# Performance work log

Measured on AMD Instinct MI355X. Metric: run time of the kernel, lower is better.

Reference implementation:

```python
import jax, jax.numpy as jnp
import numpy as np

B, S, D_MODEL, H = 2, 2048, 1024, 16
D_K = D_MODEL // H
THETA = 10000.0


def setup_inputs() -> dict:
    key = jax.random.key(0)
    k1, k2, k3 = jax.random.split(key, 3)
    x = jax.random.normal(k1, (B, S, D_MODEL), dtype=jnp.float32)
    token_positions = jnp.tile(jnp.arange(S, dtype=jnp.int32), (B, 1))
    qkv_w = jax.random.normal(k2, (3 * D_MODEL, D_MODEL), dtype=jnp.float32) * (D_MODEL ** -0.5)
    out_w = jax.random.normal(k3, (D_MODEL, D_MODEL), dtype=jnp.float32) * (D_MODEL ** -0.5)
    return {"x": x, "token_positions": token_positions, "qkv_w": qkv_w, "out_w": out_w}


def _apply_rope(t, pos):
    # t: [B, H, S, d_k], pos: [B, S]
    half = D_K // 2
    inv_freq = THETA ** (-jnp.arange(0, half, dtype=jnp.float32) * 2.0 / D_K)  # [half]
    ang = pos.astype(jnp.float32)[:, None, :, None] * inv_freq  # [B,1,S,half]
    cos, sin = jnp.cos(ang), jnp.sin(ang)
    t1 = t[..., 0::2]
    t2 = t[..., 1::2]
    r1 = t1 * cos - t2 * sin
    r2 = t1 * sin + t2 * cos
    # interleave back: [..., half, 2] -> [..., d_k]
    return jnp.stack([r1, r2], axis=-1).reshape(t.shape)


def reference(x, token_positions, qkv_w, out_w):
    # fused QKV projection (no bias)
    qkv = jnp.einsum('bsd,ed->bse', x, qkv_w)  # [B,S,3*D_MODEL]
    qkv = qkv.reshape(B, S, 3, H, D_K)
    q = jnp.transpose(qkv[:, :, 0], (0, 2, 1, 3))  # [B,H,S,d_k]
    k = jnp.transpose(qkv[:, :, 1], (0, 2, 1, 3))
    v = jnp.transpose(qkv[:, :, 2], (0, 2, 1, 3))
    q = _apply_rope(q, token_positions)
    k = _apply_rope(k, token_positions)
    scores = jnp.einsum('bhqd,bhkd->bhqk', q, k) / jnp.sqrt(jnp.asarray(D_K, x.dtype))
    causal = jnp.tril(jnp.ones((S, S), dtype=bool))
    neg_inf = jnp.finfo(scores.dtype).min
    scores = jnp.where(causal, scores, neg_inf)
    attn = jax.nn.softmax(scores, axis=-1)
    out = jnp.einsum('bhqk,bhkd->bhqd', attn, v)  # [B,H,S,d_k]
    out = jnp.transpose(out, (0, 2, 1, 3)).reshape(B, S, D_MODEL)
    return jnp.einsum('bsd,ed->bse', out, out_w)
```

## Files before the change

### kernel.cpp

```cpp
#include <hip/hip_runtime.h>
#include <cstdint>

typedef unsigned short u16;
typedef unsigned int u32;
typedef __attribute__((ext_vector_type(8))) short short8;
typedef __attribute__((ext_vector_type(4))) float f32x4;

static constexpr int Bc = 2, Sc = 2048, DMc = 1024, Hc = 16, DKc = 64;
static constexpr int Mc = Bc * Sc;
static constexpr int BHSc = Bc * Hc * Sc;

__device__ __forceinline__ float b2f(u16 u) { return __uint_as_float((u32)u << 16); }
__device__ __forceinline__ u16 f2b(float f) {
  u32 x = __float_as_uint(f);
  return (u16)((x + 0x7fffu + ((x >> 16) & 1u)) >> 16);
}
__device__ __forceinline__ u32 pack2(float lo, float hi) {
  return (u32)f2b(lo) | ((u32)f2b(hi) << 16);
}

__global__ __launch_bounds__(256)
void cvt3_k(const float* __restrict__ x, const float* __restrict__ qw,
            const float* __restrict__ ow,
            u16* __restrict__ xb, u16* __restrict__ qwb, u16* __restrict__ owb)
{
  const int i = blockIdx.x * 256 + threadIdx.x;
  const float* src; u16* dst; int j;
  if (i < 524288)      { src = x;  dst = xb;  j = i; }
  else if (i < 917504) { src = qw; dst = qwb; j = i - 524288; }
  else                 { src = ow; dst = owb; j = i - 917504; }
  const float4 a = *(const float4*)(src + (size_t)j * 8);
  const float4 b = *(const float4*)(src + (size_t)j * 8 + 4);
  uint4 o;
  o.x = pack2(a.x, a.y);
  o.y = pack2(a.z, a.w);
  o.z = pack2(b.x, b.y);
  o.w = pack2(b.z, b.w);
  *(uint4*)(dst + (size_t)j * 8) = o;
}

template <typename OutT>
__global__ __launch_bounds__(256, 2)
void gemm_bt128(const u16* __restrict__ A, const u16* __restrict__ W,
                OutT* __restrict__ C, int M, int N, int K)
{
  __shared__ u16 As[128 * 32];
  __shared__ u16 Bs[128 * 32];
  const int t = threadIdx.x;
  const int w = t >> 6, l = t & 63;
  const int wr = w >> 1, wc = w & 1;
  const int l4 = l >> 4, l15 = l & 15;
  const int bm = blockIdx.x, bn = blockIdx.y;

  f32x4 acc[4][4] = {};

  const int rowA = bm * 128, rowB = bn * 128;
  const int sr = l >> 2, sk = (l & 3) * 8;

  for (int k0 = 0; k0 < K; k0 += 32) {
    __syncthreads();
#pragma unroll
    for (int i = 0; i < 2; ++i) {
      const int chunk = i * 4 + w;
      const u16* ga = A + (size_t)(rowA + chunk * 16 + sr) * K + k0 + sk;
      const u16* gb = W + (size_t)(rowB + chunk * 16 + sr) * K + k0 + sk;
      __builtin_amdgcn_global_load_lds((const __attribute__((address_space(1))) void*)ga,
                                       (__attribute__((address_space(3))) void*)(As + chunk * 512), 16, 0, 0);
      __builtin_amdgcn_global_load_lds((const __attribute__((address_space(1))) void*)gb,
                                       (__attribute__((address_space(3))) void*)(Bs + chunk * 512), 16, 0, 0);
    }
    __syncthreads();
    short8 af[4], bf[4];
#pragma unroll
    for (int m = 0; m < 4; ++m)
      af[m] = *(const short8*)(As + (wr * 64 + m * 16 + l15) * 32 + l4 * 8);
#pragma unroll
    for (int n = 0; n < 4; ++n)
      bf[n] = *(const short8*)(Bs + (wc * 64 + n * 16 + l15) * 32 + l4 * 8);
#pragma unroll
    for (int m = 0; m < 4; ++m)
#pragma unroll
      for (int n = 0; n < 4; ++n)
        acc[m][n] = __builtin_amdgcn_mfma_f32_16x16x32_bf16(af[m], bf[n], acc[m][n], 0, 0, 0);
  }

#pragma unroll
  for (int m = 0; m < 4; ++m) {
    const int r0 = rowA + wr * 64 + m * 16 + l4 * 4;
#pragma unroll
    for (int n = 0; n < 4; ++n) {
      const int c0 = rowB + wc * 64 + n * 16 + l15;
#pragma unroll
      for (int r = 0; r < 4; ++r) {
        const float v = acc[m][n][r];
        if constexpr (sizeof(OutT) == 2)
          C[(size_t)(r0 + r) * N + c0] = (OutT)f2b(v);
        else
          C[(size_t)(r0 + r) * N + c0] = (OutT)v;
      }
    }
  }
}

__global__ void rope_table_k(float2* __restrict__ tab)
{
  const int idx = blockIdx.x * 256 + threadIdx.x;
  const int p = idx >> 5, i = idx & 31;
  const float invf = powf(10000.0f, -(float)(2 * i) / 64.0f);
  const float ang = (float)p * invf;
  tab[idx] = make_float2(cosf(ang), sinf(ang));
}

__global__ __launch_bounds__(256)
void rope_reshape_k(const u16* __restrict__ qkv, const int* __restrict__ tokpos,
                    const float2* __restrict__ tab,
                    u16* __restrict__ Q, u16* __restrict__ K, u16* __restrict__ Vt)
{
  __shared__ u16 Vs[64][72];
  const int t = threadIdx.x;
  const int st = blockIdx.x, h = blockIdx.y, b = blockIdx.z;

  {
    const int sl = t >> 2, iq = t & 3;
    const int s = st * 64 + sl;
    const int p = tokpos[b * Sc + s];
    const size_t row = (size_t)(b * Sc + s) * 3 * DMc + h * DKc + iq * 16;
    const size_t orow = ((size_t)(b * Hc + h) * Sc + s) * DKc + iq * 16;
#pragma unroll
    for (int which = 0; which < 2; ++which) {
      const u16* g = qkv + row + which * DMc;
      uint4 va = *(const uint4*)g;
      uint4 vb = *(const uint4*)(g + 8);
      u32 in[8] = {va.x, va.y, va.z, va.w, vb.x, vb.y, vb.z, vb.w};
      const float scale = (which == 0) ? 0.125f : 1.0f;
      u32 ow[8];
#pragma unroll
      for (int j = 0; j < 8; ++j) {
        const float2 cs = tab[p * 32 + iq * 8 + j];
        const float t1 = b2f((u16)(in[j] & 0xffffu));
        const float t2 = b2f((u16)(in[j] >> 16));
        ow[j] = pack2((t1 * cs.x - t2 * cs.y) * scale, (t1 * cs.y + t2 * cs.x) * scale);
      }
      u16* dst = (which == 0 ? Q : K) + orow;
      *(uint4*)dst = make_uint4(ow[0], ow[1], ow[2], ow[3]);
      *(uint4*)(dst + 8) = make_uint4(ow[4], ow[5], ow[6], ow[7]);
    }
  }
#pragma unroll
  for (int it = 0; it < 2; ++it) {
    const int sv = it * 32 + (t >> 3);
    const int d0 = (t & 7) * 8;
    const u16* g = qkv + (size_t)(b * Sc + st * 64 + sv) * 3 * DMc + 2 * DMc + h * DKc + d0;
    *(uint4*)&Vs[sv][d0] = *(const uint4*)g;
  }
  __syncthreads();
  {
    const int d = t >> 2, s0 = (t & 3) * 16;
    u16 tmp[16];
#pragma unroll
    for (int j = 0; j < 16; ++j) tmp[j] = Vs[s0 + j][d];
    u16* dst = Vt + ((size_t)(b * Hc + h) * DKc + d) * Sc + st * 64 + s0;
    *(uint4*)dst = *(const uint4*)tmp;
    *(uint4*)(dst + 8) = *(const uint4*)(tmp + 8);
  }
}

__global__ __launch_bounds__(256, 4)
void attn_k(const u16* __restrict__ Q, const u16* __restrict__ K,
            const u16* __restrict__ Vt, float* __restrict__ Opart,
            float2* __restrict__ ML)
{
  __shared__ u16 Kls[2][64 * 64];
  __shared__ u16 Vls[2][64 * 64];

  const int t = threadIdx.x, w = t >> 6, l = t & 63;
  const int l4 = l >> 4, l15 = l & 15;

  int bid = blockIdx.x;
  bid = (bid & 7) * 128 + (bid >> 3);
  const int p = bid & 15, part = (bid >> 4) & 1, h = (bid >> 5) & 15, b = bid >> 9;

  const int bh = b * Hc + h;
  const u16* Qb = Q + (size_t)bh * Sc * DKc;
  const u16* Kb = K + (size_t)bh * Sc * DKc;
  const u16* Vb = Vt + (size_t)bh * DKc * Sc;
  const int swz = (l15 & 7) << 4;

  const int qt0 = 31 - p, qt1 = p;
  const int q00 = qt0 * 64 + w * 16, q01 = qt1 * 64 + w * 16;
  const int n0 = (qt0 + 2 - part) >> 1, n1 = (qt1 + 2 - part) >> 1;
  const int ntot = n0 + n1;

  const short8 qf0a = *(const short8*)(Qb + (size_t)(q00 + l15) * DKc + l4 * 8);
  const short8 qf0b = *(const short8*)(Qb + (size_t)(q00 + l15) * DKc + 32 + l4 * 8);
  const short8 qf1a = *(const short8*)(Qb + (size_t)(q01 + l15) * DKc + l4 * 8);
  const short8 qf1b = *(const short8*)(Qb + (size_t)(q01 + l15) * DKc + 32 + l4 * 8);

  int srow[2], scol[2];
#pragma unroll
  for (int j = 0; j < 2; ++j) {
    const int e = j * 256 + t;
    srow[j] = e >> 3;
    scol[j] = (((e & 7) * 16) ^ ((srow[j] & 7) << 4)) >> 1;
  }
  auto stage = [&](int buf, int kv0) {
#pragma unroll
    for (int j = 0; j < 2; ++j) {
      const u16* gk = Kb + (size_t)(kv0 + srow[j]) * DKc + scol[j];
      __builtin_amdgcn_global_load_lds((const __attribute__((address_space(1))) void*)gk,
          (__attribute__((address_space(3))) void*)(&Kls[buf][0] + (j * 256 + w * 64) * 8), 16, 0, 0);
    }
#pragma unroll
    for (int j = 0; j < 2; ++j) {
      const u16* gv = Vb + (size_t)srow[j] * Sc + kv0 + scol[j];
      __builtin_amdgcn_global_load_lds((const __attribute__((address_space(1))) void*)gv,
          (__attribute__((address_space(3))) void*)(&Vls[buf][0] + (j * 256 + w * 64) * 8), 16, 0, 0);
    }
  };
  auto kvof = [&](int i) {
    return ((i < n0) ? (part + 2 * i) : (part + 2 * (i - n0))) * 64;
  };

  f32x4 o[4] = {};
  float m = -1e30f, lsum = 0.f;
  int qcur = q00;
  short8 qfA = qf0a, qfB = qf0b;

  auto epi = [&](int qbase) {
    const size_t pbase = ((size_t)part * Bc * Hc + bh) * Sc;
    if (l < 16) ML[pbase + qbase + l15] = make_float2(m, lsum);
#pragma unroll
    for (int dc = 0; dc < 4; ++dc)
#pragma unroll
      for (int r = 0; r < 4; ++r)
        Opart[(pbase + qbase + l4 * 4 + r) * 64 + dc * 16 + l15] = o[dc][r];
  };

  stage(0, kvof(0));
  for (int i = 0; i < ntot; ++i) {
    const int buf = i & 1;
    const int kv0 = kvof(i);
    if (i + 1 < ntot) {
      stage(buf ^ 1, kvof(i + 1));
      asm volatile("s_waitcnt vmcnt(4)" ::: "memory");
    } else {
      asm volatile("s_waitcnt vmcnt(0)" ::: "memory");
    }
    __builtin_amdgcn_s_barrier();

    const char* Kbuf = (const char*)&Kls[buf][0];
    const char* Vbuf = (const char*)&Vls[buf][0];
    char* Pw = (char*)&Kls[buf][0] + w * 2048;

    f32x4 sc[4];
#pragma unroll
    for (int c = 0; c < 4; ++c) {
      const int rb = (c * 16 + l15) * 128;
      const short8 ka  = *(const short8*)(Kbuf + rb + ((l4 * 16) ^ swz));
      const short8 kb2 = *(const short8*)(Kbuf + rb + ((64 + l4 * 16) ^ swz));
      f32x4 z = {0.f, 0.f, 0.f, 0.f};
      z = __builtin_amdgcn_mfma_f32_16x16x32_bf16(ka, qfA, z, 0, 0, 0);
      z = __builtin_amdgcn_mfma_f32_16x16x32_bf16(kb2, qfB, z, 0, 0, 0);
      sc[c] = z;
    }
    if (kv0 + 63 > qcur) {
#pragma unroll
      for (int c = 0; c < 4; ++c) {
        const int kvr = kv0 + c * 16 + l4 * 4;
#pragma unroll
        for (int r = 0; r < 4; ++r)
          if (kvr + r > qcur + l15) sc[c][r] = -1e30f;
      }
    }
    float pmax = -1e30f;
#pragma unroll
    for (int c = 0; c < 4; ++c)
      pmax = fmaxf(pmax, fmaxf(fmaxf(sc[c][0], sc[c][1]), fmaxf(sc[c][2], sc[c][3])));
    pmax = fmaxf(pmax, __shfl_xor(pmax, 16));
    pmax = fmaxf(pmax, __shfl_xor(pmax, 32));
    const float mnew = fmaxf(m, pmax);
    const float fac = __expf(m - mnew);
    float rs = 0.f;
    u32 pk[4][2];
#pragma unroll
    for (int c = 0; c < 4; ++c) {
      const float p0 = __expf(sc[c][0] - mnew);
      const float p1 = __expf(sc[c][1] - mnew);
      const float p2 = __expf(sc[c][2] - mnew);
      const float p3 = __expf(sc[c][3] - mnew);
      rs += (p0 + p1) + (p2 + p3);
      pk[c][0] = pack2(p0, p1);
      pk[c][1] = pack2(p2, p3);
    }
    rs += __shfl_xor(rs, 16);
    rs += __shfl_xor(rs, 32);
    lsum = lsum * fac + rs;
    m = mnew;

    asm volatile("s_waitcnt lgkmcnt(0)" ::: "memory");
    __builtin_amdgcn_s_barrier();

#pragma unroll
    for (int c = 0; c < 4; ++c) {
      uint2 u; u.x = pk[c][0]; u.y = pk[c][1];
      *(uint2*)(Pw + ((l15 * 128 + c * 32 + l4 * 8) ^ swz)) = u;
    }
    float f4[4];
#pragma unroll
    for (int r = 0; r < 4; ++r) f4[r] = __shfl(fac, l4 * 4 + r);
#pragma unroll
    for (int dc = 0; dc < 4; ++dc) {
      o[dc][0] *= f4[0]; o[dc][1] *= f4[1];
      o[dc][2] *= f4[2]; o[dc][3] *= f4[3];
    }
#pragma unroll
    for (int kv2 = 0; kv2 < 2; ++kv2) {
      const short8 pa = *(const short8*)(Pw + ((l15 * 128 + kv2 * 64 + l4 * 16) ^ swz));
#pragma unroll
      for (int dc = 0; dc < 4; ++dc) {
        const short8 vf = *(const short8*)(Vbuf + (dc * 16 + l15) * 128 + ((kv2 * 64 + l4 * 16) ^ swz));
        o[dc] = __builtin_amdgcn_mfma_f32_16x16x32_bf16(pa, vf, o[dc], 0, 0, 0);
      }
    }
    asm volatile("s_waitcnt lgkmcnt(0)" ::: "memory");
    __builtin_amdgcn_s_barrier();

    if (i == n0 - 1) {
      epi(q00);
#pragma unroll
      for (int dc = 0; dc < 4; ++dc) o[dc] = f32x4{0.f, 0.f, 0.f, 0.f};
      m = -1e30f; lsum = 0.f;
      qcur = q01; qfA = qf1a; qfB = qf1b;
    }
  }
  epi(q01);
}

__global__ __launch_bounds__(256)
void combine_k(const float* __restrict__ Opart, const float2* __restrict__ ML,
               u16* __restrict__ Oa)
{
  const int idx = blockIdx.x * 256 + threadIdx.x;
  const int row = idx >> 4, c4 = idx & 15;
  const float2 a = ML[row], bm = ML[BHSc + row];
  const float m = fmaxf(a.x, bm.x);
  const float w0 = __expf(a.x - m), w1 = __expf(bm.x - m);
  const float inv = 1.0f / (w0 * a.y + w1 * bm.y);
  const float4 o0 = *(const float4*)(Opart + (size_t)row * 64 + c4 * 4);
  const float4 o1 = *(const float4*)(Opart + ((size_t)BHSc + row) * 64 + c4 * 4);
  const float r0 = (w0 * o0.x + w1 * o1.x) * inv;
  const float r1 = (w0 * o0.y + w1 * o1.y) * inv;
  const float r2 = (w0 * o0.z + w1 * o1.z) * inv;
  const float r3 = (w0 * o0.w + w1 * o1.w) * inv;
  const int s = row & (Sc - 1), bh = row >> 11, b = bh >> 4, h = bh & 15;
  uint2 pk;
  pk.x = pack2(r0, r1);
  pk.y = pack2(r2, r3);
  *(uint2*)(Oa + ((size_t)(b * Sc + s) * DMc + h * DKc + c4 * 4)) = pk;
}

extern "C" void kernel_launch(void* const* d_in, const int* in_sizes, int n_in,
                              void* d_out, int out_size, void* d_ws, size_t ws_size,
                              hipStream_t stream)
{
  const float* x      = (const float*)d_in[0];
  const int*   tokpos = (const int*)d_in[1];
  const float* qkv_w  = (const float*)d_in[2];
  const float* out_w  = (const float*)d_in[3];
  float* out = (float*)d_out;

  char* ws = (char*)d_ws;
  size_t off = 0;
  u16*   qkv   = (u16*)(ws + off);
  u16*   xb    = (u16*)(ws + off + 25165824);
  u16*   qwb   = (u16*)(ws + off + 33554432);
  float* Opart = (float*)(ws + off);
  float2* ML   = (float2*)(ws + off + 33554432);
  off += 39845888;
  u16* owb = (u16*)(ws + off); off += (size_t)DMc * DMc * 2;
  u16* Qr  = (u16*)(ws + off); off += (size_t)Bc * Hc * Sc * DKc * 2;
  u16* Kr  = (u16*)(ws + off); off += (size_t)Bc * Hc * Sc * DKc * 2;
  u16* Vt  = (u16*)(ws + off); off += (size_t)Bc * Hc * DKc * Sc * 2;
  u16* Oa  = (u16*)(ws + off); off += (size_t)Mc * DMc * 2;
  float2* tab = (float2*)(ws + off); off += (size_t)Sc * 32 * sizeof(float2);

  cvt3_k<<<4096, 256, 0, stream>>>(x, qkv_w, out_w, xb, qwb, owb);
  rope_table_k<<<(Sc * 32) / 256, 256, 0, stream>>>(tab);
  gemm_bt128<u16><<<dim3(Mc / 128, 3 * DMc / 128), 256, 0, stream>>>(xb, qwb, qkv, Mc, 3 * DMc, DMc);
  rope_reshape_k<<<dim3(Sc / 64, Hc, Bc), 256, 0, stream>>>(qkv, tokpos, tab, Qr, Kr, Vt);
  attn_k<<<1024, 256, 0, stream>>>(Qr, Kr, Vt, Opart, ML);
  combine_k<<<BHSc * 16 / 256, 256, 0, stream>>>(Opart, ML, Oa);
  gemm_bt128<float><<<dim3(Mc / 128, DMc / 128), 256, 0, stream>>>(Oa, owb, out, Mc, DMc, DMc);
}
```

Baseline: 134.5 us.

## Use exp2 softmax with lazy rescale, hardware bf16 packing, and MFMA priority hints

Folds log2(e) into the Q scale so the softmax can use the native exp2 instruction everywhere, including the combine kernel. Rescaling of the output accumulator and running sum is skipped unless some row's max grows by more than a threshold, which removes per-tile multiplies and shuffles. Software round-to-nearest bf16 packing is replaced by the v_cvt_pk_bf16_f32 instruction, and s_setprio is raised around the MFMA blocks. Lazy rescaling lets unnormalised probabilities reach up to 2^8, so the bf16 P values and fp32 sums carry a somewhat larger dynamic range.

```diff
diff --git a/kernel.cpp b/kernel.cpp
--- a/kernel.cpp
+++ b/kernel.cpp
@@ -10,6 +10,12 @@
 static constexpr int Mc = Bc * Sc;
 static constexpr int BHSc = Bc * Hc * Sc;
 
+#if __has_builtin(__builtin_amdgcn_exp2f)
+#define EXP2F(x) __builtin_amdgcn_exp2f(x)
+#else
+#define EXP2F(x) exp2f(x)
+#endif
+
 __device__ __forceinline__ float b2f(u16 u) { return __uint_as_float((u32)u << 16); }
 __device__ __forceinline__ u16 f2b(float f) {
   u32 x = __float_as_uint(f);
@@ -17,6 +23,11 @@
 }
 __device__ __forceinline__ u32 pack2(float lo, float hi) {
   return (u32)f2b(lo) | ((u32)f2b(hi) << 16);
+}
+__device__ __forceinline__ u32 cvtpk(float lo, float hi) {
+  u32 r;
+  asm("v_cvt_pk_bf16_f32 %0, %1, %2" : "=v"(r) : "v"(lo), "v"(hi));
+  return r;
 }
 
 __global__ __launch_bounds__(256)
@@ -32,10 +43,10 @@
   const float4 a = *(const float4*)(src + (size_t)j * 8);
   const float4 b = *(const float4*)(src + (size_t)j * 8 + 4);
   uint4 o;
-  o.x = pack2(a.x, a.y);
-  o.y = pack2(a.z, a.w);
-  o.z = pack2(b.x, b.y);
-  o.w = pack2(b.z, b.w);
+  o.x = cvtpk(a.x, a.y);
+  o.y = cvtpk(a.z, a.w);
+  o.z = cvtpk(b.x, b.y);
+  o.w = cvtpk(b.z, b.w);
   *(uint4*)(dst + (size_t)j * 8) = o;
 }
 
@@ -132,14 +143,14 @@
       uint4 va = *(const uint4*)g;
       uint4 vb = *(const uint4*)(g + 8);
       u32 in[8] = {va.x, va.y, va.z, va.w, vb.x, vb.y, vb.z, vb.w};
-      const float scale = (which == 0) ? 0.125f : 1.0f;
+      const float scale = (which == 0) ? 0.18033688011112f : 1.0f;
       u32 ow[8];
 #pragma unroll
       for (int j = 0; j < 8; ++j) {
         const float2 cs = tab[p * 32 + iq * 8 + j];
         const float t1 = b2f((u16)(in[j] & 0xffffu));
         const float t2 = b2f((u16)(in[j] >> 16));
-        ow[j] = pack2((t1 * cs.x - t2 * cs.y) * scale, (t1 * cs.y + t2 * cs.x) * scale);
+        ow[j] = cvtpk((t1 * cs.x - t2 * cs.y) * scale, (t1 * cs.y + t2 * cs.x) * scale);
       }
       u16* dst = (which == 0 ? Q : K) + orow;
       *(uint4*)dst = make_uint4(ow[0], ow[1], ow[2], ow[3]);
@@ -253,6 +264,7 @@
     char* Pw = (char*)&Kls[buf][0] + w * 2048;
 
     f32x4 sc[4];
+    __builtin_amdgcn_s_setprio(1);
 #pragma unroll
     for (int c = 0; c < 4; ++c) {
       const int rb = (c * 16 + l15) * 128;
@@ -263,6 +275,7 @@
       z = __builtin_amdgcn_mfma_f32_16x16x32_bf16(kb2, qfB, z, 0, 0, 0);
       sc[c] = z;
     }
+    __builtin_amdgcn_s_setprio(0);
     if (kv0 + 63 > qcur) {
 #pragma unroll
       for (int c = 0; c < 4; ++c) {
@@ -278,24 +291,35 @@
       pmax = fmaxf(pmax, fmaxf(fmaxf(sc[c][0], sc[c][1]), fmaxf(sc[c][2], sc[c][3])));
     pmax = fmaxf(pmax, __shfl_xor(pmax, 16));
     pmax = fmaxf(pmax, __shfl_xor(pmax, 32));
-    const float mnew = fmaxf(m, pmax);
-    const float fac = __expf(m - mnew);
+    if (!__all(pmax - m <= 8.0f)) {
+      const float mnew = fmaxf(m, pmax);
+      const float fac = EXP2F(m - mnew);
+      float f4[4];
+#pragma unroll
+      for (int r = 0; r < 4; ++r) f4[r] = __shfl(fac, l4 * 4 + r);
+#pragma unroll
+      for (int dc = 0; dc < 4; ++dc) {
+        o[dc][0] *= f4[0]; o[dc][1] *= f4[1];
+        o[dc][2] *= f4[2]; o[dc][3] *= f4[3];
+      }
+      lsum *= fac;
+      m = mnew;
+    }
     float rs = 0.f;
     u32 pk[4][2];
 #pragma unroll
     for (int c = 0; c < 4; ++c) {
-      const float p0 = __expf(sc[c][0] - mnew);
-      const float p1 = __expf(sc[c][1] - mnew);
-      const float p2 = __expf(sc[c][2] - mnew);
-      const float p3 = __expf(sc[c][3] - mnew);
+      const float p0 = EXP2F(sc[c][0] - m);
+      const float p1 = EXP2F(sc[c][1] - m);
+      const float p2 = EXP2F(sc[c][2] - m);
+      const float p3 = EXP2F(sc[c][3] - m);
       rs += (p0 + p1) + (p2 + p3);
-      pk[c][0] = pack2(p0, p1);
-      pk[c][1] = pack2(p2, p3);
+      pk[c][0] = cvtpk(p0, p1);
+      pk[c][1] = cvtpk(p2, p3);
     }
     rs += __shfl_xor(rs, 16);
     rs += __shfl_xor(rs, 32);
-    lsum = lsum * fac + rs;
-    m = mnew;
+    lsum += rs;
 
     asm volatile("s_waitcnt lgkmcnt(0)" ::: "memory");
     __builtin_amdgcn_s_barrier();
@@ -305,14 +329,7 @@
       uint2 u; u.x = pk[c][0]; u.y = pk[c][1];
       *(uint2*)(Pw + ((l15 * 128 + c * 32 + l4 * 8) ^ swz)) = u;
     }
-    float f4[4];
-#pragma unroll
-    for (int r = 0; r < 4; ++r) f4[r] = __shfl(fac, l4 * 4 + r);
-#pragma unroll
-    for (int dc = 0; dc < 4; ++dc) {
-      o[dc][0] *= f4[0]; o[dc][1] *= f4[1];
-      o[dc][2] *= f4[2]; o[dc][3] *= f4[3];
-    }
+    __builtin_amdgcn_s_setprio(1);
 #pragma unroll
     for (int kv2 = 0; kv2 < 2; ++kv2) {
       const short8 pa = *(const short8*)(Pw + ((l15 * 128 + kv2 * 64 + l4 * 16) ^ swz));
@@ -322,6 +339,7 @@
         o[dc] = __builtin_amdgcn_mfma_f32_16x16x32_bf16(pa, vf, o[dc], 0, 0, 0);
       }
     }
+    __builtin_amdgcn_s_setprio(0);
     asm volatile("s_waitcnt lgkmcnt(0)" ::: "memory");
     __builtin_amdgcn_s_barrier();
 
@@ -344,7 +362,7 @@
   const int row = idx >> 4, c4 = idx & 15;
   const float2 a = ML[row], bm = ML[BHSc + row];
   const float m = fmaxf(a.x, bm.x);
-  const float w0 = __expf(a.x - m), w1 = __expf(bm.x - m);
+  const float w0 = EXP2F(a.x - m), w1 = EXP2F(bm.x - m);
   const float inv = 1.0f / (w0 * a.y + w1 * bm.y);
   const float4 o0 = *(const float4*)(Opart + (size_t)row * 64 + c4 * 4);
   const float4 o1 = *(const float4*)(Opart + ((size_t)BHSc + row) * 64 + c4 * 4);
@@ -354,8 +372,8 @@
   const float r3 = (w0 * o0.w + w1 * o1.w) * inv;
   const int s = row & (Sc - 1), bh = row >> 11, b = bh >> 4, h = bh & 15;
   uint2 pk;
-  pk.x = pack2(r0, r1);
-  pk.y = pack2(r2, r3);
+  pk.x = cvtpk(r0, r1);
+  pk.y = cvtpk(r2, r3);
   *(uint2*)(Oa + ((size_t)(b * Sc + s) * DMc + h * DKc + c4 * 4)) = pk;
 }
 
```

Result: faster. 125.9 us (-6.3%).
